# Kernel tuning notes

Measured on AMD Instinct MI355X. Metric: run time of the kernel, lower is better.

## Reference

```python
import jax, jax.numpy as jnp
import numpy as np

D = 1024
H = 16
DH = D // H
B, T = 2, 2048


def setup_inputs() -> dict:
    key = jax.random.key(0)
    ks = jax.random.split(key, 5)
    x = jax.random.normal(ks[0], (B, T, D), dtype=jnp.float32)
    # torch nn.Linear init scale ~ 1/sqrt(fan_in)
    sc = 1.0 / np.sqrt(D)
    W_qkv = jax.random.uniform(ks[1], (3 * D, D), dtype=jnp.float32, minval=-sc, maxval=sc)
    b_qkv = jax.random.uniform(ks[2], (3 * D,), dtype=jnp.float32, minval=-sc, maxval=sc)
    W_o = jax.random.uniform(ks[3], (D, D), dtype=jnp.float32, minval=-sc, maxval=sc)
    b_o = jax.random.uniform(ks[4], (D,), dtype=jnp.float32, minval=-sc, maxval=sc)
    return {"x": x, "W_qkv": W_qkv, "b_qkv": b_qkv, "W_o": W_o, "b_o": b_o}


def reference(x, W_qkv, b_qkv, W_o, b_o):
    Bx, Tx, C = x.shape
    scale = DH ** -0.5
    qkv = x @ W_qkv.T + b_qkv                       # [B,T,3D]
    qkv = qkv.reshape(Bx, Tx, 3, H, DH)
    q, k, v = jnp.moveaxis(qkv, 2, 0)               # each [B,T,H,DH]
    q = q.transpose(0, 2, 1, 3)                     # [B,H,T,DH]
    k = k.transpose(0, 2, 1, 3)
    v = v.transpose(0, 2, 1, 3)
    scores = jnp.einsum("bhqd,bhkd->bhqk", q, k) * scale
    a = jax.nn.softmax(scores, axis=-1)
    o = jnp.einsum("bhqk,bhkd->bhqd", a, v)         # [B,H,T,DH]
    o = o.transpose(0, 2, 1, 3).reshape(Bx, Tx, C)
    return o @ W_o.T + b_o
```

## Files before the change

### kernel.cpp

```cpp
#include <hip/hip_runtime.h>

#define TT 2048
#define DD 1024
#define HH 16
#define DHH 64

typedef __attribute__((ext_vector_type(4)))  float  f32x4;
typedef __attribute__((ext_vector_type(16))) float  f32x16;
typedef __attribute__((ext_vector_type(8)))  short  bf16x8;
typedef __attribute__((ext_vector_type(4)))  float  f4;
typedef __attribute__((ext_vector_type(4)))  unsigned short u16x4;
typedef __attribute__((ext_vector_type(4)))  unsigned int   u32x4;

__device__ __forceinline__ unsigned short f2b(float f) {
    union { float f; unsigned int u; } v; v.f = f;
    unsigned int r = v.u + 0x7fffu + ((v.u >> 16) & 1u);
    return (unsigned short)(r >> 16);
}

__device__ __forceinline__ void gl_lds16(const void* g, void* l) {
    __builtin_amdgcn_global_load_lds(
        (const __attribute__((address_space(1))) unsigned int*)g,
        (__attribute__((address_space(3))) unsigned int*)l, 16, 0, 0);
}

__device__ __forceinline__ f32x16 mfma32(bf16x8 a, bf16x8 b, f32x16 c) {
    return __builtin_amdgcn_mfma_f32_32x32x16_bf16(a, b, c, 0, 0, 0);
}

__device__ __forceinline__ float fexp2(float x) {
    float r; asm("v_exp_f32 %0, %1" : "=v"(r) : "v"(x)); return r;
}

__device__ __forceinline__ unsigned int pkbf(float a, float b) {
    unsigned int r;
    asm("v_cvt_pk_bf16_f32 %0, %1, %2" : "=v"(r) : "v"(a), "v"(b));
    return r;
}

__device__ __forceinline__ void pl32swap(unsigned int& a, unsigned int& b) {
    asm("v_permlane32_swap_b32 %0, %1" : "+v"(a), "+v"(b));
}

__device__ __forceinline__ bf16x8 u2h(u32x4 u) {
    union { u32x4 u; bf16x8 h; } x; x.u = u; return x.h;
}

__global__ void f2b_kernel(const float* __restrict__ s, unsigned short* __restrict__ d, int n4) {
    int i = blockIdx.x * blockDim.x + threadIdx.x;
    int stride = gridDim.x * blockDim.x;
    for (; i < n4; i += stride) {
        f4 v = ((const f4*)s)[i];
        u16x4 o;
        o[0] = f2b(v[0]); o[1] = f2b(v[1]); o[2] = f2b(v[2]); o[3] = f2b(v[3]);
        ((u16x4*)d)[i] = o;
    }
}

template<int BN, int MODE>
__global__ __launch_bounds__(256) void gemm_bt(
    const unsigned short* __restrict__ A, const unsigned short* __restrict__ Bm,
    const float* __restrict__ bias, int N, int K,
    unsigned short* __restrict__ q, unsigned short* __restrict__ k,
    unsigned short* __restrict__ vt, float* __restrict__ outf)
{
    constexpr int NB  = BN / 32;
    constexpr int ASZ = 128 * 32;
    constexpr int BSZ = BN * 32;
    __shared__ unsigned short lds[2 * (ASZ + BSZ)];

    int tid = threadIdx.x;
    int l = tid & 63, w = tid >> 6;
    int wr = w >> 1, wc = w & 1;
    int lr = l & 15, lk = (l >> 4) * 8;
    int bm = blockIdx.y, bn = blockIdx.x;

    f32x4 acc[4][NB] = {};

    const unsigned short* Ag = A + (size_t)(bm * 128) * K;
    const unsigned short* Bg = Bm + (size_t)(bn * BN) * K;

    auto stage = [&](int buf, int k0) {
        unsigned short* As = lds + buf * (ASZ + BSZ);
        unsigned short* Bs = As + ASZ;
#pragma unroll
        for (int r = 0; r < 2; ++r) {
            int e = r * 256 + tid;
            int row = e >> 2, kc = (e & 3) * 8;
            gl_lds16(Ag + (size_t)row * K + k0 + kc, &As[e * 8]);
        }
#pragma unroll
        for (int r = 0; r < BN / 64; ++r) {
            int e = r * 256 + tid;
            int row = e >> 2, kc = (e & 3) * 8;
            gl_lds16(Bg + (size_t)row * K + k0 + kc, &Bs[e * 8]);
        }
    };

    stage(0, 0);
    __syncthreads();
    int cur = 0;
    for (int k0 = 0; k0 < K; k0 += 32) {
        if (k0 + 32 < K) stage(cur ^ 1, k0 + 32);
        const unsigned short* As = lds + cur * (ASZ + BSZ);
        const unsigned short* Bs = As + ASZ;
        bf16x8 a[4], b[NB];
#pragma unroll
        for (int i = 0; i < 4; ++i)
            a[i] = *(const bf16x8*)&As[(wr * 64 + i * 16 + lr) * 32 + lk];
#pragma unroll
        for (int j = 0; j < NB; ++j)
            b[j] = *(const bf16x8*)&Bs[(wc * (BN / 2) + j * 16 + lr) * 32 + lk];
        __builtin_amdgcn_s_setprio(1);
#pragma unroll
        for (int i = 0; i < 4; ++i)
#pragma unroll
            for (int j = 0; j < NB; ++j)
                acc[i][j] = __builtin_amdgcn_mfma_f32_16x16x32_bf16(a[i], b[j], acc[i][j], 0, 0, 0);
        __builtin_amdgcn_s_setprio(0);
        __syncthreads();
        cur ^= 1;
    }

#pragma unroll
    for (int i = 0; i < 4; ++i) {
#pragma unroll
        for (int j = 0; j < NB; ++j) {
            int row0 = bm * 128 + wr * 64 + i * 16 + (l >> 4) * 4;
            int col  = bn * BN + wc * (BN / 2) + j * 16 + (l & 15);
            float bv = bias[col];
#pragma unroll
            for (int r = 0; r < 4; ++r) {
                float val = acc[i][j][r] + bv;
                int m = row0 + r;
                if (MODE == 0) {
                    int which = col >> 10, rem = col & 1023;
                    int h = rem >> 6, d = rem & 63;
                    int b = m >> 11, t = m & 2047;
                    if (which == 0) {
                        q[((size_t)((b * HH + h) * TT + t)) * DHH + d] = f2b(val * 0.18033688011112042f);
                    } else if (which == 1) {
                        k[((size_t)((b * HH + h) * TT + t)) * DHH + d] = f2b(val);
                    } else {
                        vt[((size_t)((b * HH + h) * DHH + d)) * TT + t] = f2b(val);
                    }
                } else {
                    outf[(size_t)m * N + col] = val;
                }
            }
        }
    }
}

__global__ __launch_bounds__(256) void attn(
    const unsigned short* __restrict__ qb,
    const unsigned short* __restrict__ kb,
    const unsigned short* __restrict__ vtb,
    unsigned short* __restrict__ ob)
{
    extern __shared__ char lds[];

    int tid = threadIdx.x;
    int l = tid & 63, w = tid >> 6;
    int hi = l >> 5, c = l & 31;

    int lin = blockIdx.y * gridDim.x + blockIdx.x;
    int swz = (lin & 7) * 64 + (lin >> 3);
    int bh = swz >> 4;
    int qrow = (swz & 15) * 128 + w * 32 + c;

    bf16x8 qf[4];
    const unsigned short* qg = qb + ((size_t)bh * TT + qrow) * DHH;
#pragma unroll
    for (int kd = 0; kd < 4; ++kd)
        qf[kd] = *(const bf16x8*)(qg + kd * 16 + hi * 8);

    f32x16 oa0 = {}, oa1 = {};
    float m = -1e30f, lsum = 0.f;

    const char* kgl = (const char*)(kb + (size_t)bh * TT * DHH);
    const char* vgl = (const char*)(vtb + (size_t)bh * DHH * TT);

    auto stage = [&](int buf, int kt0) {
        char* base = lds + buf * 32768;
#pragma unroll
        for (int r = 0; r < 4; ++r) {
            int p = r * 4096 + tid * 16;
            {
                int rw = p >> 7, qq = p & 127;
                int sw = qq ^ ((rw & 7) << 4);
                gl_lds16(kgl + (size_t)(kt0 + rw) * 128 + sw, base + p);
            }
            {
                int rw = p >> 8, qq = p & 255;
                int sw = qq ^ ((rw & 7) << 4);
                gl_lds16(vgl + (size_t)rw * (TT * 2) + kt0 * 2 + sw, base + 16384 + p);
            }
        }
    };

    stage(0, 0);
    __syncthreads();
    int cur = 0;

    for (int kt0 = 0; kt0 < TT; kt0 += 128) {
        if (kt0 + 128 < TT) stage(cur ^ 1, kt0 + 128);
        const char* Ksb = lds + cur * 32768;
        const char* Vsb = Ksb + 16384;

#pragma unroll
        for (int kbi = 0; kbi < 2; ++kbi) {
            f32x16 s0 = {}, s1 = {};
            __builtin_amdgcn_s_setprio(1);
#pragma unroll
            for (int kd = 0; kd < 4; ++kd) {
                int cb = (kd * 16 + hi * 8) * 2;
                int xr = cb ^ ((c & 7) << 4);
                bf16x8 kf0 = *(const bf16x8*)(Ksb + (kbi * 64 + c) * 128 + xr);
                bf16x8 kf1 = *(const bf16x8*)(Ksb + (kbi * 64 + 32 + c) * 128 + xr);
                s0 = mfma32(kf0, qf[kd], s0);
                s1 = mfma32(kf1, qf[kd], s1);
            }
            __builtin_amdgcn_s_setprio(0);

            float mx[16];
#pragma unroll
            for (int r = 0; r < 16; ++r) mx[r] = fmaxf(s0[r], s1[r]);
#pragma unroll
            for (int d = 8; d >= 1; d >>= 1)
#pragma unroll
                for (int r = 0; r < d; ++r) mx[r] = fmaxf(mx[r], mx[r + d]);
            float tm = fmaxf(mx[0], __shfl_xor(mx[0], 32, 64));

            float nm = fmaxf(m, tm);
            if (!__all(nm - m <= 8.f)) {
                float corr = fexp2(m - nm);
                lsum *= corr;
#pragma unroll
                for (int r = 0; r < 16; ++r) { oa0[r] *= corr; oa1[r] *= corr; }
                m = nm;
            }

            float p4[4] = {0.f, 0.f, 0.f, 0.f};
#pragma unroll
            for (int r = 0; r < 16; ++r) { s0[r] = fexp2(s0[r] - m); p4[r & 3] += s0[r]; }
#pragma unroll
            for (int r = 0; r < 16; ++r) { s1[r] = fexp2(s1[r] - m); p4[r & 3] += s1[r]; }
            float psum = (p4[0] + p4[1]) + (p4[2] + p4[3]);
            psum += __shfl_xor(psum, 32);
            lsum += psum;

            u32x4 pf0, pf1, pf2, pf3;
#define MKFRAG(sv, base_, dst) { \
            unsigned int c0 = pkbf(sv[base_+0], sv[base_+1]); \
            unsigned int c1 = pkbf(sv[base_+2], sv[base_+3]); \
            unsigned int c2 = pkbf(sv[base_+4], sv[base_+5]); \
            unsigned int c3 = pkbf(sv[base_+6], sv[base_+7]); \
            pl32swap(c0, c2); pl32swap(c1, c3); \
            dst[0] = c0; dst[1] = c1; dst[2] = c2; dst[3] = c3; }
            MKFRAG(s0, 0, pf0)
            MKFRAG(s0, 8, pf1)
            MKFRAG(s1, 0, pf2)
            MKFRAG(s1, 8, pf3)
#undef MKFRAG

            __builtin_amdgcn_s_setprio(1);
#define PVSTEP(kc, pf) { \
            int cb = kbi * 128 + (kc * 16 + hi * 8) * 2; \
            int xr = ((c & 7) << 4); \
            bf16x8 vf0 = *(const bf16x8*)(Vsb + c * 256 + (cb ^ xr)); \
            bf16x8 vf1 = *(const bf16x8*)(Vsb + (32 + c) * 256 + (cb ^ xr)); \
            bf16x8 ph = u2h(pf); \
            oa0 = mfma32(vf0, ph, oa0); \
            oa1 = mfma32(vf1, ph, oa1); }
            PVSTEP(0, pf0)
            PVSTEP(1, pf1)
            PVSTEP(2, pf2)
            PVSTEP(3, pf3)
#undef PVSTEP
            __builtin_amdgcn_s_setprio(0);
        }

        __syncthreads();
        cur ^= 1;
    }

    float rn = 1.0f / lsum;
    int b = bh >> 4, h = bh & 15;
    unsigned short* obase = ob + ((size_t)(b * TT + qrow)) * DD + h * 64;
#pragma unroll
    for (int g = 0; g < 4; ++g) {
        u16x4 o0, o1;
#pragma unroll
        for (int e = 0; e < 4; ++e) {
            o0[e] = f2b(oa0[g * 4 + e] * rn);
            o1[e] = f2b(oa1[g * 4 + e] * rn);
        }
        *(u16x4*)(obase + 8 * g + 4 * hi)      = o0;
        *(u16x4*)(obase + 32 + 8 * g + 4 * hi) = o1;
    }
}

extern "C" void kernel_launch(void* const* d_in, const int* in_sizes, int n_in,
                              void* d_out, int out_size, void* d_ws, size_t ws_size,
                              hipStream_t stream) {
    const float* x    = (const float*)d_in[0];
    const float* Wqkv = (const float*)d_in[1];
    const float* bqkv = (const float*)d_in[2];
    const float* Wo   = (const float*)d_in[3];
    const float* bo   = (const float*)d_in[4];
    float* out = (float*)d_out;

    unsigned short* xb  = (unsigned short*)d_ws;
    unsigned short* wqb = xb  + 4096 * 1024;
    unsigned short* wob = wqb + 3072 * 1024;
    unsigned short* q   = wob + 1024 * 1024;
    unsigned short* k   = q   + 2 * 16 * 2048 * 64;
    unsigned short* vt  = k   + 2 * 16 * 2048 * 64;
    unsigned short* ob  = vt  + 2 * 16 * 2048 * 64;

    f2b_kernel<<<dim3(1024), dim3(256), 0, stream>>>(x,    xb,  4096 * 1024 / 4);
    f2b_kernel<<<dim3(768),  dim3(256), 0, stream>>>(Wqkv, wqb, 3072 * 1024 / 4);
    f2b_kernel<<<dim3(256),  dim3(256), 0, stream>>>(Wo,   wob, 1024 * 1024 / 4);

    gemm_bt<128, 0><<<dim3(24, 32), dim3(256), 0, stream>>>(xb, wqb, bqkv, 3072, 1024,
                                                            q, k, vt, nullptr);
    attn<<<dim3(16, 32), dim3(256), 65536, stream>>>(q, k, vt, ob);

    gemm_bt<64, 1><<<dim3(16, 32), dim3(256), 0, stream>>>(ob, wob, bo, 1024, 1024,
                                                           nullptr, nullptr, nullptr, out);
}
```

Measured before the change: 131.3 us.

## Split attention KV range across two wave groups with LDS merge

The attention kernel now runs 512 threads per block as two groups of four waves. Each group processes half of the key/value sequence for the same 128 query rows, and the two partial softmax states (m, lsum, O accumulators) are merged through LDS at the end. Per-group tiles shrink to 64 keys, and the double-buffered prefetch is replaced by single-buffer load, sync, compute, sync. LDS per block drops from 64KB to about 34KB, aiming for more resident waves and more parallelism per query tile, at the cost of exposed load latency and a merge step.

```diff
diff --git a/kernel.cpp b/kernel.cpp
--- a/kernel.cpp
+++ b/kernel.cpp
@@ -152,7 +152,7 @@
     }
 }
 
-__global__ __launch_bounds__(256) void attn(
+__global__ __launch_bounds__(512, 4) void attn(
     const unsigned short* __restrict__ qb,
     const unsigned short* __restrict__ kb,
     const unsigned short* __restrict__ vtb,
@@ -162,12 +162,14 @@
 
     int tid = threadIdx.x;
     int l = tid & 63, w = tid >> 6;
+    int g = w >> 2, wg = w & 3;
     int hi = l >> 5, c = l & 31;
-
-    int lin = blockIdx.y * gridDim.x + blockIdx.x;
+    int tig = tid & 255;
+
+    int lin = blockIdx.x;
     int swz = (lin & 7) * 64 + (lin >> 3);
     int bh = swz >> 4;
-    int qrow = (swz & 15) * 128 + w * 32 + c;
+    int qrow = (swz & 15) * 128 + wg * 32 + c;
 
     bf16x8 qf[4];
     const unsigned short* qg = qb + ((size_t)bh * TT + qrow) * DHH;
@@ -178,126 +180,131 @@
     f32x16 oa0 = {}, oa1 = {};
     float m = -1e30f, lsum = 0.f;
 
-    const char* kgl = (const char*)(kb + (size_t)bh * TT * DHH);
-    const char* vgl = (const char*)(vtb + (size_t)bh * DHH * TT);
-
-    auto stage = [&](int buf, int kt0) {
-        char* base = lds + buf * 32768;
-#pragma unroll
-        for (int r = 0; r < 4; ++r) {
-            int p = r * 4096 + tid * 16;
-            {
-                int rw = p >> 7, qq = p & 127;
-                int sw = qq ^ ((rw & 7) << 4);
-                gl_lds16(kgl + (size_t)(kt0 + rw) * 128 + sw, base + p);
-            }
-            {
-                int rw = p >> 8, qq = p & 255;
-                int sw = qq ^ ((rw & 7) << 4);
-                gl_lds16(vgl + (size_t)rw * (TT * 2) + kt0 * 2 + sw, base + 16384 + p);
-            }
-        }
-    };
-
-    stage(0, 0);
+    const char* kgl = (const char*)(kb + (size_t)bh * TT * DHH) + (size_t)g * 1024 * 128;
+    const char* vgl = (const char*)(vtb + (size_t)bh * DHH * TT) + (size_t)g * 1024 * 2;
+    char* base = lds + g * 16384;
+
+    for (int kt0 = 0; kt0 < 1024; kt0 += 64) {
+#pragma unroll
+        for (int r = 0; r < 2; ++r) {
+            int p = r * 4096 + tig * 16;
+            int rw = p >> 7, qq = p & 127;
+            int sw = qq ^ ((rw & 7) << 4);
+            gl_lds16(kgl + (size_t)(kt0 + rw) * 128 + sw, base + p);
+            gl_lds16(vgl + (size_t)rw * (TT * 2) + kt0 * 2 + sw, base + 8192 + p);
+        }
+        __syncthreads();
+        const char* Ksb = base;
+        const char* Vsb = base + 8192;
+
+        f32x16 s0 = {}, s1 = {};
+        __builtin_amdgcn_s_setprio(1);
+#pragma unroll
+        for (int kd = 0; kd < 4; ++kd) {
+            int cb = (kd * 16 + hi * 8) * 2;
+            int xr = cb ^ ((c & 7) << 4);
+            bf16x8 kf0 = *(const bf16x8*)(Ksb + c * 128 + xr);
+            bf16x8 kf1 = *(const bf16x8*)(Ksb + (32 + c) * 128 + xr);
+            s0 = mfma32(kf0, qf[kd], s0);
+            s1 = mfma32(kf1, qf[kd], s1);
+        }
+        __builtin_amdgcn_s_setprio(0);
+
+        float mx[16];
+#pragma unroll
+        for (int r = 0; r < 16; ++r) mx[r] = fmaxf(s0[r], s1[r]);
+#pragma unroll
+        for (int d = 8; d >= 1; d >>= 1)
+#pragma unroll
+            for (int r = 0; r < d; ++r) mx[r] = fmaxf(mx[r], mx[r + d]);
+        float tm = fmaxf(mx[0], __shfl_xor(mx[0], 32, 64));
+
+        float nm = fmaxf(m, tm);
+        if (!__all(nm - m <= 8.f)) {
+            float corr = fexp2(m - nm);
+            lsum *= corr;
+#pragma unroll
+            for (int r = 0; r < 16; ++r) { oa0[r] *= corr; oa1[r] *= corr; }
+            m = nm;
+        }
+
+        float p4[4] = {0.f, 0.f, 0.f, 0.f};
+#pragma unroll
+        for (int r = 0; r < 16; ++r) { s0[r] = fexp2(s0[r] - m); p4[r & 3] += s0[r]; }
+#pragma unroll
+        for (int r = 0; r < 16; ++r) { s1[r] = fexp2(s1[r] - m); p4[r & 3] += s1[r]; }
+        float psum = (p4[0] + p4[1]) + (p4[2] + p4[3]);
+        psum += __shfl_xor(psum, 32);
+        lsum += psum;
+
+        u32x4 pf0, pf1, pf2, pf3;
+#define MKFRAG(sv, base_, dst) { \
+        unsigned int c0 = pkbf(sv[base_+0], sv[base_+1]); \
+        unsigned int c1 = pkbf(sv[base_+2], sv[base_+3]); \
+        unsigned int c2 = pkbf(sv[base_+4], sv[base_+5]); \
+        unsigned int c3 = pkbf(sv[base_+6], sv[base_+7]); \
+        pl32swap(c0, c2); pl32swap(c1, c3); \
+        dst[0] = c0; dst[1] = c1; dst[2] = c2; dst[3] = c3; }
+        MKFRAG(s0, 0, pf0)
+        MKFRAG(s0, 8, pf1)
+        MKFRAG(s1, 0, pf2)
+        MKFRAG(s1, 8, pf3)
+#undef MKFRAG
+
+        __builtin_amdgcn_s_setprio(1);
+#define PVSTEP(kc, pf) { \
+        int cb = (kc * 16 + hi * 8) * 2; \
+        int xr = ((c & 7) << 4); \
+        bf16x8 vf0 = *(const bf16x8*)(Vsb + c * 128 + (cb ^ xr)); \
+        bf16x8 vf1 = *(const bf16x8*)(Vsb + (32 + c) * 128 + (cb ^ xr)); \
+        bf16x8 ph = u2h(pf); \
+        oa0 = mfma32(vf0, ph, oa0); \
+        oa1 = mfma32(vf1, ph, oa1); }
+        PVSTEP(0, pf0)
+        PVSTEP(1, pf1)
+        PVSTEP(2, pf2)
+        PVSTEP(3, pf3)
+#undef PVSTEP
+        __builtin_amdgcn_s_setprio(0);
+
+        __syncthreads();
+    }
+
+    float* Om = (float*)lds;
+    float* ml = (float*)(lds + 32768);
+    if (g == 1) {
+        float* o = Om + wg * 2048 + l;
+#pragma unroll
+        for (int r = 0; r < 16; ++r) o[r * 64]        = oa0[r];
+#pragma unroll
+        for (int r = 0; r < 16; ++r) o[(16 + r) * 64] = oa1[r];
+        ml[wg * 128 + l]      = m;
+        ml[wg * 128 + 64 + l] = lsum;
+    }
     __syncthreads();
-    int cur = 0;
-
-    for (int kt0 = 0; kt0 < TT; kt0 += 128) {
-        if (kt0 + 128 < TT) stage(cur ^ 1, kt0 + 128);
-        const char* Ksb = lds + cur * 32768;
-        const char* Vsb = Ksb + 16384;
-
-#pragma unroll
-        for (int kbi = 0; kbi < 2; ++kbi) {
-            f32x16 s0 = {}, s1 = {};
-            __builtin_amdgcn_s_setprio(1);
-#pragma unroll
-            for (int kd = 0; kd < 4; ++kd) {
-                int cb = (kd * 16 + hi * 8) * 2;
-                int xr = cb ^ ((c & 7) << 4);
-                bf16x8 kf0 = *(const bf16x8*)(Ksb + (kbi * 64 + c) * 128 + xr);
-                bf16x8 kf1 = *(const bf16x8*)(Ksb + (kbi * 64 + 32 + c) * 128 + xr);
-                s0 = mfma32(kf0, qf[kd], s0);
-                s1 = mfma32(kf1, qf[kd], s1);
-            }
-            __builtin_amdgcn_s_setprio(0);
-
-            float mx[16];
-#pragma unroll
-            for (int r = 0; r < 16; ++r) mx[r] = fmaxf(s0[r], s1[r]);
-#pragma unroll
-            for (int d = 8; d >= 1; d >>= 1)
-#pragma unroll
-                for (int r = 0; r < d; ++r) mx[r] = fmaxf(mx[r], mx[r + d]);
-            float tm = fmaxf(mx[0], __shfl_xor(mx[0], 32, 64));
-
-            float nm = fmaxf(m, tm);
-            if (!__all(nm - m <= 8.f)) {
-                float corr = fexp2(m - nm);
-                lsum *= corr;
-#pragma unroll
-                for (int r = 0; r < 16; ++r) { oa0[r] *= corr; oa1[r] *= corr; }
-                m = nm;
-            }
-
-            float p4[4] = {0.f, 0.f, 0.f, 0.f};
-#pragma unroll
-            for (int r = 0; r < 16; ++r) { s0[r] = fexp2(s0[r] - m); p4[r & 3] += s0[r]; }
-#pragma unroll
-            for (int r = 0; r < 16; ++r) { s1[r] = fexp2(s1[r] - m); p4[r & 3] += s1[r]; }
-            float psum = (p4[0] + p4[1]) + (p4[2] + p4[3]);
-            psum += __shfl_xor(psum, 32);
-            lsum += psum;
-
-            u32x4 pf0, pf1, pf2, pf3;
-#define MKFRAG(sv, base_, dst) { \
-            unsigned int c0 = pkbf(sv[base_+0], sv[base_+1]); \
-            unsigned int c1 = pkbf(sv[base_+2], sv[base_+3]); \
-            unsigned int c2 = pkbf(sv[base_+4], sv[base_+5]); \
-            unsigned int c3 = pkbf(sv[base_+6], sv[base_+7]); \
-            pl32swap(c0, c2); pl32swap(c1, c3); \
-            dst[0] = c0; dst[1] = c1; dst[2] = c2; dst[3] = c3; }
-            MKFRAG(s0, 0, pf0)
-            MKFRAG(s0, 8, pf1)
-            MKFRAG(s1, 0, pf2)
-            MKFRAG(s1, 8, pf3)
-#undef MKFRAG
-
-            __builtin_amdgcn_s_setprio(1);
-#define PVSTEP(kc, pf) { \
-            int cb = kbi * 128 + (kc * 16 + hi * 8) * 2; \
-            int xr = ((c & 7) << 4); \
-            bf16x8 vf0 = *(const bf16x8*)(Vsb + c * 256 + (cb ^ xr)); \
-            bf16x8 vf1 = *(const bf16x8*)(Vsb + (32 + c) * 256 + (cb ^ xr)); \
-            bf16x8 ph = u2h(pf); \
-            oa0 = mfma32(vf0, ph, oa0); \
-            oa1 = mfma32(vf1, ph, oa1); }
-            PVSTEP(0, pf0)
-            PVSTEP(1, pf1)
-            PVSTEP(2, pf2)
-            PVSTEP(3, pf3)
-#undef PVSTEP
-            __builtin_amdgcn_s_setprio(0);
-        }
-
-        __syncthreads();
-        cur ^= 1;
-    }
-
-    float rn = 1.0f / lsum;
+    if (g == 1) return;
+
+    float m2 = ml[wg * 128 + l];
+    float l2 = ml[wg * 128 + 64 + l];
+    float M  = fmaxf(m, m2);
+    float a1 = fexp2(m - M), a2 = fexp2(m2 - M);
+    float L  = lsum * a1 + l2 * a2;
+    float rn = 1.0f / L;
+    const float* o2 = Om + wg * 2048 + l;
+
     int b = bh >> 4, h = bh & 15;
     unsigned short* obase = ob + ((size_t)(b * TT + qrow)) * DD + h * 64;
 #pragma unroll
-    for (int g = 0; g < 4; ++g) {
+    for (int gq = 0; gq < 4; ++gq) {
         u16x4 o0, o1;
 #pragma unroll
         for (int e = 0; e < 4; ++e) {
-            o0[e] = f2b(oa0[g * 4 + e] * rn);
-            o1[e] = f2b(oa1[g * 4 + e] * rn);
-        }
-        *(u16x4*)(obase + 8 * g + 4 * hi)      = o0;
-        *(u16x4*)(obase + 32 + 8 * g + 4 * hi) = o1;
+            int r = gq * 4 + e;
+            o0[e] = f2b((oa0[r] * a1 + o2[r * 64] * a2) * rn);
+            o1[e] = f2b((oa1[r] * a1 + o2[(16 + r) * 64] * a2) * rn);
+        }
+        *(u16x4*)(obase + 8 * gq + 4 * hi)      = o0;
+        *(u16x4*)(obase + 32 + 8 * gq + 4 * hi) = o1;
     }
 }
 
@@ -325,7 +332,7 @@
 
     gemm_bt<128, 0><<<dim3(24, 32), dim3(256), 0, stream>>>(xb, wqb, bqkv, 3072, 1024,
                                                             q, k, vt, nullptr);
-    attn<<<dim3(16, 32), dim3(256), 65536, stream>>>(q, k, vt, ob);
+    attn<<<dim3(512), dim3(512), 34816, stream>>>(q, k, vt, ob);
 
     gemm_bt<64, 1><<<dim3(16, 32), dim3(256), 0, stream>>>(ob, wob, bo, 1024, 1024,
                                                            nullptr, nullptr, nullptr, out);
```

After: 123.8 us. -5.7%, faster.
